# Kernel optimization log

Measured on AMD Instinct MI355X. Metric: run time of the kernel, lower is better.

Reference implementation:

```python
import jax, jax.numpy as jnp
import numpy as np

KERNEL_WIDTH = 0.05      # Gaussian KDE bandwidth (Angstrom)
B_SCAT = 5.803           # neutron scattering length of O (fm)
N_ATOMS = 1024
BOX_L = 25.0
N_BINS = 400


def _trapz(y, x):
    # trapezoidal rule along last axis; x is 1D
    dx = x[1:] - x[:-1]
    return jnp.sum((y[..., 1:] + y[..., :-1]) * 0.5 * dx, axis=-1)


def setup_inputs() -> dict:
    key = jax.random.key(0)
    k1, _ = jax.random.split(key)
    positions = jax.random.uniform(k1, (N_ATOMS, 3), dtype=jnp.float32) * BOX_L
    cell = jnp.eye(3, dtype=jnp.float32) * BOX_L
    r_bins = jnp.linspace(0.1, 10.0, N_BINS, dtype=jnp.float32)
    q_bins = jnp.linspace(0.5, 25.0, N_BINS, dtype=jnp.float32)
    return {"positions": positions, "cell": cell, "r_bins": r_bins, "q_bins": q_bins}


def reference(positions, cell, r_bins, q_bins):
    w = KERNEL_WIDTH
    b = B_SCAT
    N = positions.shape[0]

    # --- minimum-image pairwise distances, upper triangle only (self-pairs) ---
    ii, jj = np.triu_indices(N, k=1)                 # static index sets, P = N(N-1)/2
    diff = positions[jj] - positions[ii]             # (P, 3), matches points_2 - points_1
    cell_inv = jnp.linalg.inv(cell)
    frac = diff @ cell_inv                            # (P, 3) fractional coords
    frac = frac - jnp.round(frac)                     # minimum image convention
    mip = frac @ cell
    d = jnp.sqrt(jnp.sum(mip * mip, axis=-1) + 1e-10)  # (P,) observed distances

    # --- Gaussian KDE binning with window mask (mask == exact exclusion) ---
    min_bin = jnp.min(r_bins) - 3.0 * w
    max_bin = jnp.max(r_bins) + 3.0 * w
    in_win = (d > min_bin) & (d < max_bin)            # (P,)
    norm = 1.0 / (w * jnp.sqrt(2.0 * jnp.pi))
    gauss = jnp.exp(-0.5 * ((r_bins[None, :] - d[:, None]) / w) ** 2) * norm  # (P, n_r)
    summed = jnp.sum(jnp.where(in_win[:, None], gauss, 0.0), axis=0)          # (n_r,)

    vol = jnp.abs(jnp.linalg.det(cell))
    n_pairs = d.shape[0]
    g_partial = vol / n_pairs * summed / (4.0 * jnp.pi * r_bins ** 2)

    # single species: frac=1, coeff = b*b*0.01; G(r) = coeff * (g_partial - 1)
    G = (b * b * 0.01) * (g_partial - 1.0)

    # --- S(Q) = 1 + 4*pi*rho/Q * int r G(r) sin(Qr) dr ---
    rho = N / vol
    integrand = (r_bins[None, :] * G[None, :] *
                 jnp.sin(q_bins[:, None] * r_bins[None, :]) /
                 (q_bins[:, None] + 1e-10))           # (n_q, n_r)
    S = 1.0 + 4.0 * jnp.pi * rho * _trapz(integrand, r_bins)

    # --- F(Q) = Q (S(Q) - 1) ---
    F = q_bins * (S - 1.0)

    return jnp.stack([G, S, F])  # (3, n_bins)
```

## Files before the change

### kernel.cpp

```cpp
#include <hip/hip_runtime.h>
#include <math.h>

#define NBINS_MAX 512
#define NMAX      1024
#define NSLOT     8
constexpr float KW       = 0.05f;
constexpr float INV_KW   = 20.0f;
constexpr float GNORM    = 0.3989422804014327f * INV_KW;
constexpr float COEFF    = 0.33674809f;
constexpr float FOUR_PI  = 12.566370614359172f;
constexpr float W5       = 5.0f * KW;
constexpr float QSCALE     = 1048576.0f;
constexpr float INV_QSCALE = 1.0f / QSCALE;
#define SENT32  (NBINS_MAX * NSLOT)


__global__ void __launch_bounds__(512)
scatter_kernel(const float* __restrict__ pos,
               const float* __restrict__ cell,
               const float* __restrict__ rbins,
               unsigned int* __restrict__ slots,
               int N, int nbins)
{
    __shared__ float sh_pos[3 * NMAX];
    __shared__ float sh_hist[NBINS_MAX];
    const int t  = threadIdx.x;
    const int nb = blockDim.x;

    const int nflt = 3 * N;
    const int nvec = nflt >> 2;
    const float4* p4 = (const float4*)pos;
    for (int v = t; v < nvec; v += nb) {
        const float4 x = p4[v];
        sh_pos[4*v + 0] = x.x;
        sh_pos[4*v + 1] = x.y;
        sh_pos[4*v + 2] = x.z;
        sh_pos[4*v + 3] = x.w;
    }
    for (int s = (nvec << 2) + t; s < nflt; s += nb)
        sh_pos[s] = pos[s];
    for (int k = t; k < nbins; k += nb)
        sh_hist[k] = 0.0f;

    float cm[9];
#pragma unroll
    for (int k = 0; k < 9; ++k) cm[k] = cell[k];
    const float a00 = cm[0], a01 = cm[1], a02 = cm[2];
    const float a10 = cm[3], a11 = cm[4], a12 = cm[5];
    const float a20 = cm[6], a21 = cm[7], a22 = cm[8];
    const float det = a00*(a11*a22 - a12*a21)
                    - a01*(a10*a22 - a12*a20)
                    + a02*(a10*a21 - a11*a20);
    const float id = 1.0f / det;
    float im[9];
    im[0] = (a11*a22 - a12*a21)*id;
    im[1] = (a02*a21 - a01*a22)*id;
    im[2] = (a01*a12 - a02*a11)*id;
    im[3] = (a12*a20 - a10*a22)*id;
    im[4] = (a00*a22 - a02*a20)*id;
    im[5] = (a02*a10 - a00*a12)*id;
    im[6] = (a10*a21 - a11*a20)*id;
    im[7] = (a01*a20 - a00*a21)*id;
    im[8] = (a00*a11 - a01*a10)*id;

    const float r0     = rbins[0];
    const float rend   = rbins[nbins - 1];
    const float minb   = r0   - 3.0f * KW;
    const float maxb   = rend + 3.0f * KW;
    const float dr     = (rend - r0) / (float)(nbins - 1);
    const float inv_dr = 1.0f / dr;
    const int   WB     = (int)(W5 * inv_dr) + 1;
    const float du     = dr * INV_KW;
    const float hdu2   = 0.5f * du * du;
    const float m2     = __expf(-du * du);

    __syncthreads();

    const int nrp = (N + 1) / 2;
    const int rp0 = 2 * blockIdx.x;

    auto do_rowpair = [&](int rp) {
        const int A    = rp;
        const int B    = N - 1 - rp;
        const int cntA = N - 1 - A;
        const int cntB = (B != A) ? A : 0;
        const int tot  = cntA + cntB;
        for (int p = t; p < tot; p += nb) {
            int i, j;
            if (p < cntA) { i = A; j = A + 1 + p; }
            else          { i = B; j = B + 1 + (p - cntA); }

            const float dx = sh_pos[3*j + 0] - sh_pos[3*i + 0];
            const float dy = sh_pos[3*j + 1] - sh_pos[3*i + 1];
            const float dz = sh_pos[3*j + 2] - sh_pos[3*i + 2];
            float fx = dx*im[0] + dy*im[3] + dz*im[6];
            float fy = dx*im[1] + dy*im[4] + dz*im[7];
            float fz = dx*im[2] + dy*im[5] + dz*im[8];
            fx -= rintf(fx); fy -= rintf(fy); fz -= rintf(fz);
            const float mx = fx*cm[0] + fy*cm[3] + fz*cm[6];
            const float my = fx*cm[1] + fy*cm[4] + fz*cm[7];
            const float mz = fx*cm[2] + fy*cm[5] + fz*cm[8];
            const float d  = sqrtf(mx*mx + my*my + mz*mz + 1e-10f);

            if (d > minb && d < maxb) {
                const int kc  = (int)((d - r0) * inv_dr);
                int klo = kc - WB; if (klo < 0)         klo = 0;
                int khi = kc + WB; if (khi > nbins - 1) khi = nbins - 1;
                const float rlo = fmaf((float)klo, dr, r0);
                const float u0  = (rlo - d) * INV_KW;
                float e = __expf(-0.5f * u0 * u0);
                float g = __expf(-(u0 * du + hdu2));
                for (int k = klo; k <= khi; ++k) {
                    atomicAdd(&sh_hist[k], e);
                    e *= g;
                    g *= m2;
                }
            }
        }
    };
    do_rowpair(rp0);
    if (rp0 + 1 < nrp) do_rowpair(rp0 + 1);

    __syncthreads();
    const int slot = blockIdx.x & (NSLOT - 1);
    for (int k = t; k < nbins; k += nb) {
        const unsigned int q = (unsigned int)rintf(sh_hist[k] * QSCALE);
        if (q) atomicAdd(&slots[k * NSLOT + slot], q);
    }
}

__global__ void __launch_bounds__(256)
spectrum_kernel(const unsigned int* __restrict__ slots,
                const float* __restrict__ cell,
                const float* __restrict__ rbins,
                const float* __restrict__ qbins,
                float* __restrict__ out,
                int N, int nbins)
{
    __shared__ float  sh_r[NBINS_MAX];
    __shared__ float2 sh_w2[NBINS_MAX];
    __shared__ float  sh_red[4];
    const int t = threadIdx.x;

    const unsigned int base = slots[SENT32];

    const float a00 = cell[0], a01 = cell[1], a02 = cell[2];
    const float a10 = cell[3], a11 = cell[4], a12 = cell[5];
    const float a20 = cell[6], a21 = cell[7], a22 = cell[8];
    const float det = a00*(a11*a22 - a12*a21)
                    - a01*(a10*a22 - a12*a20)
                    + a02*(a10*a21 - a11*a20);
    const float vol     = fabsf(det);
    const float n_pairs = 0.5f * (float)N * (float)(N - 1);
    const float rho     = (float)N / vol;
    const float pref    = (vol / n_pairs) * GNORM;

    const uint4* s4 = (const uint4*)slots;
    for (int k = t; k < nbins; k += 256) {
        const uint4 aa = s4[2*k + 0];
        const uint4 bb = s4[2*k + 1];
        unsigned long long tot = 0;
        tot += (unsigned long long)(aa.x - base);
        tot += (unsigned long long)(aa.y - base);
        tot += (unsigned long long)(aa.z - base);
        tot += (unsigned long long)(aa.w - base);
        tot += (unsigned long long)(bb.x - base);
        tot += (unsigned long long)(bb.y - base);
        tot += (unsigned long long)(bb.z - base);
        tot += (unsigned long long)(bb.w - base);
        const float summed = (float)tot * INV_QSCALE;
        const float rk = rbins[k];
        const float g  = pref * summed / (FOUR_PI * rk * rk);
        const float G  = COEFF * (g - 1.0f);
        if (blockIdx.x == 0) out[k] = G;
        sh_r[k]  = rk;
        sh_w2[k] = make_float2(G, rk);
    }
    __syncthreads();

    for (int k = t; k < nbins; k += 256) {
        const float rk   = sh_r[k];
        const float w_lo = (k > 0)         ? (rk - sh_r[k - 1]) : 0.0f;
        const float w_hi = (k < nbins - 1) ? (sh_r[k + 1] - rk) : 0.0f;
        sh_w2[k].x = 0.5f * (w_lo + w_hi) * rk * sh_w2[k].x;
    }
    __syncthreads();

    const int   qi   = blockIdx.x;
    const float q    = qbins[qi];
    const float qinv = 1.0f / (q + 1e-10f);
    float acc = 0.0f;
    for (int k = t; k < nbins; k += 256) {
        const float2 v = sh_w2[k];
        acc += v.x * __sinf(q * v.y);
    }
#pragma unroll
    for (int off = 32; off > 0; off >>= 1)
        acc += __shfl_down(acc, off, 64);
    if ((t & 63) == 0) sh_red[t >> 6] = acc;
    __syncthreads();
    if (t == 0) {
        const float S = 1.0f + FOUR_PI * rho * qinv *
                        (sh_red[0] + sh_red[1] + sh_red[2] + sh_red[3]);
        out[nbins + qi]     = S;
        out[2 * nbins + qi] = q * (S - 1.0f);
    }
}

extern "C" void kernel_launch(void* const* d_in, const int* in_sizes, int n_in,
                              void* d_out, int out_size, void* d_ws, size_t ws_size,
                              hipStream_t stream)
{
    const float* pos   = (const float*)d_in[0];
    const float* cell  = (const float*)d_in[1];
    const float* rbins = (const float*)d_in[2];
    const float* qbins = (const float*)d_in[3];
    float* out = (float*)d_out;

    const int N     = in_sizes[0] / 3;
    const int nbins = in_sizes[2];
    const int nrp   = (N + 1) / 2;
    const int grid1 = (nrp + 1) / 2;

    unsigned int* slots = (unsigned int*)d_ws;

    hipLaunchKernelGGL(scatter_kernel, dim3(grid1), dim3(512), 0, stream,
                       pos, cell, rbins, slots, N, nbins);
    hipLaunchKernelGGL(spectrum_kernel, dim3(nbins), dim3(256), 0, stream,
                       slots, cell, rbins, qbins, out, N, nbins);
}
```

Baseline: 83.47 us.

## Bin pair distances into fine LDS histogram with first-order moment, then convolve Gaussian

Instead of each in-window pair issuing about a dozen shared-memory float atomics to spread its Gaussian over nearby coarse bins, each pair now does one packed integer atomic into an 8192-entry fine histogram. The packed word holds a count and a quantized offset from the fine-bin centre. After the pair loop, each wave evaluates the Gaussian sum for one output bin over the fine bins in its window, using a first-order Taylor correction from the stored offset. This removes most per-pair LDS atomic traffic and exp work, at the cost of a 32KB LDS array, a per-block convolution pass, and approximation and quantization error (including possible overflow of the packed offset field when a fine bin holds many pairs).

```diff
diff --git a/kernel.cpp b/kernel.cpp
--- a/kernel.cpp
+++ b/kernel.cpp
@@ -3,16 +3,17 @@
 
 #define NBINS_MAX 512
 #define NMAX      1024
+#define NFINE_LDS 8192
 #define NSLOT     8
+#define SENT32  (NBINS_MAX * NSLOT)
 constexpr float KW       = 0.05f;
 constexpr float INV_KW   = 20.0f;
 constexpr float GNORM    = 0.3989422804014327f * INV_KW;
 constexpr float COEFF    = 0.33674809f;
 constexpr float FOUR_PI  = 12.566370614359172f;
-constexpr float W5       = 5.0f * KW;
+constexpr float GWIN     = 6.0f * KW;
 constexpr float QSCALE     = 1048576.0f;
 constexpr float INV_QSCALE = 1.0f / QSCALE;
-#define SENT32  (NBINS_MAX * NSLOT)
 
 
 __global__ void __launch_bounds__(512)
@@ -22,8 +23,9 @@
                unsigned int* __restrict__ slots,
                int N, int nbins)
 {
-    __shared__ float sh_pos[3 * NMAX];
-    __shared__ float sh_hist[NBINS_MAX];
+    __shared__ float        sh_pos[3 * NMAX];
+    __shared__ unsigned int sh_fm[NFINE_LDS];
+    __shared__ float        sh_coarse[NBINS_MAX];
     const int t  = threadIdx.x;
     const int nb = blockDim.x;
 
@@ -39,8 +41,8 @@
     }
     for (int s = (nvec << 2) + t; s < nflt; s += nb)
         sh_pos[s] = pos[s];
-    for (int k = t; k < nbins; k += nb)
-        sh_hist[k] = 0.0f;
+    for (int s = t; s < NFINE_LDS; s += nb)
+        sh_fm[s] = 0u;
 
     float cm[9];
 #pragma unroll
@@ -67,12 +69,11 @@
     const float rend   = rbins[nbins - 1];
     const float minb   = r0   - 3.0f * KW;
     const float maxb   = rend + 3.0f * KW;
+    const float span   = maxb + 0.1f;
+    const float fd     = span / (float)NFINE_LDS;
+    const float inv_fd = (float)NFINE_LDS / span;
+    const float rs     = 4096.0f / fd;
     const float dr     = (rend - r0) / (float)(nbins - 1);
-    const float inv_dr = 1.0f / dr;
-    const int   WB     = (int)(W5 * inv_dr) + 1;
-    const float du     = dr * INV_KW;
-    const float hdu2   = 0.5f * du * du;
-    const float m2     = __expf(-du * du);
 
     __syncthreads();
 
@@ -103,18 +104,10 @@
             const float d  = sqrtf(mx*mx + my*my + mz*mz + 1e-10f);
 
             if (d > minb && d < maxb) {
-                const int kc  = (int)((d - r0) * inv_dr);
-                int klo = kc - WB; if (klo < 0)         klo = 0;
-                int khi = kc + WB; if (khi > nbins - 1) khi = nbins - 1;
-                const float rlo = fmaf((float)klo, dr, r0);
-                const float u0  = (rlo - d) * INV_KW;
-                float e = __expf(-0.5f * u0 * u0);
-                float g = __expf(-(u0 * du + hdu2));
-                for (int k = klo; k <= khi; ++k) {
-                    atomicAdd(&sh_hist[k], e);
-                    e *= g;
-                    g *= m2;
-                }
+                const int   f  = (int)(d * inv_fd);
+                const float e  = d - ((float)f + 0.5f) * fd;
+                const int   eq = (int)rintf(e * rs);
+                atomicAdd(&sh_fm[f], (1u << 20) + (unsigned int)(eq + 4096));
             }
         }
     };
@@ -122,9 +115,43 @@
     if (rp0 + 1 < nrp) do_rowpair(rp0 + 1);
 
     __syncthreads();
+
+    const int   wave  = t >> 6;
+    const int   lane  = t & 63;
+    const int   nw    = nb >> 6;
+    const float dstep = 64.0f * fd * INV_KW;
+    const float m2    = __expf(-dstep * dstep);
+    const float c1    = fd * INV_KW / 4096.0f;
+    const int   wf    = (int)(GWIN * inv_fd) + 1;
+
+    for (int k = wave; k < nbins; k += nw) {
+        const float rk = fmaf((float)k, dr, r0);
+        const int   fc = (int)(rk * inv_fd);
+        int flo = fc - wf; if (flo < 0)             flo = 0;
+        int fhi = fc + wf; if (fhi > NFINE_LDS - 1) fhi = NFINE_LDS - 1;
+        const int f0 = flo + lane;
+        float u = (rk - ((float)f0 + 0.5f) * fd) * INV_KW;
+        float e = __expf(-0.5f * u * u);
+        float g = __expf(fmaf(u, dstep, -0.5f * dstep * dstep));
+        float acc = 0.0f;
+        for (int f = f0; f <= fhi; f += 64) {
+            const unsigned int v = sh_fm[f];
+            const float cf = (float)(v >> 20);
+            const float Rf = (float)((int)(v & 0xFFFFFu)
+                                     - (int)((v >> 20) * 4096u));
+            acc = fmaf(fmaf(u * c1, Rf, cf), e, acc);
+            u -= dstep; e *= g; g *= m2;
+        }
+#pragma unroll
+        for (int off = 32; off > 0; off >>= 1)
+            acc += __shfl_down(acc, off, 64);
+        if (lane == 0) sh_coarse[k] = acc;
+    }
+    __syncthreads();
+
     const int slot = blockIdx.x & (NSLOT - 1);
     for (int k = t; k < nbins; k += nb) {
-        const unsigned int q = (unsigned int)rintf(sh_hist[k] * QSCALE);
+        const unsigned int q = (unsigned int)rintf(sh_coarse[k] * QSCALE);
         if (q) atomicAdd(&slots[k * NSLOT + slot], q);
     }
 }
```

Result: slower. 106.5 us (+27.6%).

## Replace per-pair Gaussian scatter with fine-grid moment histogram and per-bin reconstruction

Applied to the files above, without the earlier changes.

Each pair no longer spreads about eleven Gaussian contributions across histogram bins with shared-memory float atomics. It now does a single 64-bit atomic into a fine grid (quarter bin spacing) that packs a count, a first moment and a second moment of the offset. After the pair loop, each thread rebuilds one output bin by summing a second-order Taylor-corrected Gaussian over nearby fine-grid cells. This cuts shared atomics per pair sharply but adds approximation error and a fixed per-block reconstruction cost, and the t<484 cap hardcodes the bin limit. Signed accumulation in the spectrum kernel allows for negative corrections.

```diff
diff --git a/kernel.cpp b/kernel.cpp
--- a/kernel.cpp
+++ b/kernel.cpp
@@ -3,16 +3,22 @@
 
 #define NBINS_MAX 512
 #define NMAX      1024
+#define NFG       2048
+#define GOFF      64
+#define WHALF     49
 #define NSLOT     8
+#define SENT32  (NBINS_MAX * NSLOT)
 constexpr float KW       = 0.05f;
 constexpr float INV_KW   = 20.0f;
 constexpr float GNORM    = 0.3989422804014327f * INV_KW;
 constexpr float COEFF    = 0.33674809f;
 constexpr float FOUR_PI  = 12.566370614359172f;
-constexpr float W5       = 5.0f * KW;
 constexpr float QSCALE     = 1048576.0f;
 constexpr float INV_QSCALE = 1.0f / QSCALE;
-#define SENT32  (NBINS_MAX * NSLOT)
+constexpr float ES  = 33554432.0f;
+constexpr float E2S = 536870912.0f;
+constexpr float A1  = INV_KW / ES;
+constexpr float A2  = 0.5f * INV_KW * INV_KW / E2S;
 
 
 __global__ void __launch_bounds__(512)
@@ -23,7 +29,7 @@
                int N, int nbins)
 {
     __shared__ float sh_pos[3 * NMAX];
-    __shared__ float sh_hist[NBINS_MAX];
+    __shared__ unsigned long long sh_fm[NFG];
     const int t  = threadIdx.x;
     const int nb = blockDim.x;
 
@@ -39,8 +45,8 @@
     }
     for (int s = (nvec << 2) + t; s < nflt; s += nb)
         sh_pos[s] = pos[s];
-    for (int k = t; k < nbins; k += nb)
-        sh_hist[k] = 0.0f;
+    for (int s = t; s < NFG; s += nb)
+        sh_fm[s] = 0ull;
 
     float cm[9];
 #pragma unroll
@@ -68,11 +74,8 @@
     const float minb   = r0   - 3.0f * KW;
     const float maxb   = rend + 3.0f * KW;
     const float dr     = (rend - r0) / (float)(nbins - 1);
-    const float inv_dr = 1.0f / dr;
-    const int   WB     = (int)(W5 * inv_dr) + 1;
-    const float du     = dr * INV_KW;
-    const float hdu2   = 0.5f * du * du;
-    const float m2     = __expf(-du * du);
+    const float fdelta = 0.25f * dr;
+    const float inv_fd = 1.0f / fdelta;
 
     __syncthreads();
 
@@ -103,18 +106,16 @@
             const float d  = sqrtf(mx*mx + my*my + mz*mz + 1e-10f);
 
             if (d > minb && d < maxb) {
-                const int kc  = (int)((d - r0) * inv_dr);
-                int klo = kc - WB; if (klo < 0)         klo = 0;
-                int khi = kc + WB; if (khi > nbins - 1) khi = nbins - 1;
-                const float rlo = fmaf((float)klo, dr, r0);
-                const float u0  = (rlo - d) * INV_KW;
-                float e = __expf(-0.5f * u0 * u0);
-                float g = __expf(-(u0 * du + hdu2));
-                for (int k = klo; k <= khi; ++k) {
-                    atomicAdd(&sh_hist[k], e);
-                    e *= g;
-                    g *= m2;
-                }
+                const int   gi = (int)rintf((d - r0) * inv_fd) + GOFF;
+                const float e  = d - fmaf((float)(gi - GOFF), fdelta, r0);
+                const int   eq  = (int)rintf(e * ES);
+                const unsigned int e2q = (unsigned int)rintf(e * e * E2S);
+                const unsigned long long val =
+                      (1ull << 52)
+                    | ((unsigned long long)e2q << 29)
+                    | (unsigned long long)(unsigned int)(eq + 131072);
+                const int addr = ((gi & 3) << 9) | (gi >> 2);
+                atomicAdd(&sh_fm[addr], val);
             }
         }
     };
@@ -122,10 +123,35 @@
     if (rp0 + 1 < nrp) do_rowpair(rp0 + 1);
 
     __syncthreads();
-    const int slot = blockIdx.x & (NSLOT - 1);
-    for (int k = t; k < nbins; k += nb) {
-        const unsigned int q = (unsigned int)rintf(sh_hist[k] * QSCALE);
-        if (q) atomicAdd(&slots[k * NSLOT + slot], q);
+
+    if (t < nbins && t < 484) {
+        const int   k  = t;
+        const float dw = fdelta * INV_KW;
+        float u = (float)WHALF * dw;
+        float e = __expf(-0.5f * u * u);
+        float g = __expf(fmaf(u, dw, -0.5f * dw * dw));
+        const float m = __expf(-dw * dw);
+        float acc = 0.0f;
+        const int gbase = 4 * k + GOFF - WHALF;
+#pragma unroll 4
+        for (int it = 0; it <= 2 * WHALF; ++it) {
+            const int gi   = gbase + it;
+            const int addr = ((gi & 3) << 9) | (gi >> 2);
+            const unsigned long long v = sh_fm[addr];
+            const unsigned int cntu = (unsigned int)(v >> 52);
+            const float cnt = (float)cntu;
+            const float m2  = (float)(unsigned int)((v >> 29) & 0x7FFFFFu);
+            const float m1  = (float)((int)((unsigned int)v & 0x1FFFFFFFu)
+                                      - (int)(cntu << 17));
+            const float term = fmaf(u * A1, m1,
+                               fmaf(fmaf(u, u, -1.0f) * A2, m2, cnt));
+            acc = fmaf(term, e, acc);
+            e *= g; g *= m;
+            u -= dw;
+        }
+        const int slot = blockIdx.x & (NSLOT - 1);
+        const int q = (int)rintf(acc * QSCALE);
+        if (q) atomicAdd(&slots[k * NSLOT + slot], (unsigned int)q);
     }
 }
 
@@ -159,15 +185,15 @@
     for (int k = t; k < nbins; k += 256) {
         const uint4 aa = s4[2*k + 0];
         const uint4 bb = s4[2*k + 1];
-        unsigned long long tot = 0;
-        tot += (unsigned long long)(aa.x - base);
-        tot += (unsigned long long)(aa.y - base);
-        tot += (unsigned long long)(aa.z - base);
-        tot += (unsigned long long)(aa.w - base);
-        tot += (unsigned long long)(bb.x - base);
-        tot += (unsigned long long)(bb.y - base);
-        tot += (unsigned long long)(bb.z - base);
-        tot += (unsigned long long)(bb.w - base);
+        long long tot = 0;
+        tot += (int)(aa.x - base);
+        tot += (int)(aa.y - base);
+        tot += (int)(aa.z - base);
+        tot += (int)(aa.w - base);
+        tot += (int)(bb.x - base);
+        tot += (int)(bb.y - base);
+        tot += (int)(bb.z - base);
+        tot += (int)(bb.w - base);
         const float summed = (float)tot * INV_QSCALE;
         const float rk = rbins[k];
         const float g  = pref * summed / (FOUR_PI * rk * rk);
```

Result: faster. 76.57 us (-8.3%).
